# Performance work log

Measured on AMD Instinct MI355X. Metric: run time of the kernel, lower is better.

## Reference

```python
import jax, jax.numpy as jnp
import numpy as np

DIM = 4096
N_HEADS = 32
N_KV_HEADS = 8
HEAD_DIM = 128
WINDOW = 4096
BATCH = 32
START_POS = 4095


def setup_inputs() -> dict:
    key = jax.random.key(0)
    ks = jax.random.split(key, 8)
    x = jax.random.normal(ks[0], (BATCH, DIM), dtype=jnp.float32)
    wqkv = jax.random.normal(ks[1], (DIM, (N_HEADS + 2 * N_KV_HEADS) * HEAD_DIM), dtype=jnp.float32) * 0.02
    wo = jax.random.normal(ks[2], (N_HEADS * HEAD_DIM, DIM), dtype=jnp.float32) * 0.02
    cos = jax.random.uniform(ks[3], (HEAD_DIM,), dtype=jnp.float32)
    sin = jax.random.uniform(ks[4], (HEAD_DIM,), dtype=jnp.float32)
    cache_k = jax.random.normal(ks[5], (BATCH, N_KV_HEADS, WINDOW, HEAD_DIM), dtype=jnp.float32)
    cache_v = jax.random.normal(ks[6], (BATCH, N_KV_HEADS, WINDOW, HEAD_DIM), dtype=jnp.float32)
    mask = jnp.zeros((BATCH, 1, 1, WINDOW), dtype=jnp.float32)
    return {"x": x, "wqkv": wqkv, "wo": wo, "cos": cos, "sin": sin,
            "cache_k": cache_k, "cache_v": cache_v, "mask": mask,
            "start_pos": START_POS}


def _rotate_half(t):
    t1, t2 = jnp.split(t, 2, axis=-1)
    return jnp.concatenate([-t2, t1], axis=-1)


def _rope(t, cos, sin):
    # t: [..., head_dim]; cos/sin: [head_dim] at the current decode position
    return t * cos + _rotate_half(t) * sin


def reference(x, wqkv, wo, cos, sin, cache_k, cache_v, mask, start_pos):
    B, D = x.shape
    KV = cache_k.shape[1]
    Hd = cache_k.shape[3]
    window = cache_k.shape[2]
    H = wo.shape[0] // Hd
    R = H // KV  # GQA repeats
    scale = 1.0 / np.sqrt(Hd)

    # fused QKV projection (matmul_1d + nlp_create_qkv_heads)
    qkv = x @ wqkv  # [B, (H+2*KV)*Hd]
    q = qkv[:, : H * Hd].reshape(B, H, Hd)
    k = qkv[:, H * Hd : (H + KV) * Hd].reshape(B, KV, Hd)
    v = qkv[:, (H + KV) * Hd :].reshape(B, KV, Hd)

    # rotary embedding on q and k at current position
    q = _rope(q, cos, sin)
    k = _rope(k, cos, sin)

    # sliding-window KV cache update at current_pos
    cur = start_pos % window  # python int
    cache_k = cache_k.at[:, :, cur].set(k)
    cache_v = cache_v.at[:, :, cur].set(v)

    # unpad to padded_layer_past_len = min(nearest_32(start_pos+1), window)
    padded_len = min(((start_pos + 1 + 31) // 32) * 32, window)
    keys = cache_k[:, :, :padded_len]   # [B, KV, T, Hd]
    values = cache_v[:, :, :padded_len]

    # grouped-query attention: q -> [B, KV, R, Hd]
    qg = q.reshape(B, KV, R, Hd)
    scores = jnp.einsum("bgrd,bgtd->bgrt", qg, keys) * scale  # [B, KV, R, T]
    scores = scores + mask[:, :, :, :padded_len]  # broadcast over kv-heads/repeats
    attn = jax.nn.softmax(scores, axis=-1)
    out = jnp.einsum("bgrt,bgtd->bgrd", attn, values)  # [B, KV, R, Hd]

    # concat heads + output projection
    out = out.reshape(B, H * Hd)
    return out @ wo  # [B, D]
```

## Files before the change

kernel.cpp:

```cpp
#include <hip/hip_runtime.h>
#include <math.h>

#define DIM 4096
#define NH 32
#define NKV 8
#define HD 128
#define WINDOW 4096
#define BATCH 32
#define QKV_N 6144
#define ATTN_SCALE 0.08838834764831845f
#define WCHUNK 128
#define NCW 32
#define SLICES 16

__device__ __forceinline__ float4 f4max(float4 a, float4 b) {
  return make_float4(fmaxf(a.x, b.x), fmaxf(a.y, b.y), fmaxf(a.z, b.z), fmaxf(a.w, b.w));
}
__device__ __forceinline__ float4 f4add(float4 a, float4 b) {
  return make_float4(a.x + b.x, a.y + b.y, a.z + b.z, a.w + b.w);
}
__device__ __forceinline__ void fma4(float4& a, float4 x, float4 y) {
  a.x = fmaf(x.x, y.x, a.x); a.y = fmaf(x.y, y.y, a.y);
  a.z = fmaf(x.z, y.z, a.z); a.w = fmaf(x.w, y.w, a.w);
}
__device__ __forceinline__ void fma4s(float4& a, float s, float4 v) {
  a.x = fmaf(s, v.x, a.x); a.y = fmaf(s, v.y, a.y);
  a.z = fmaf(s, v.z, a.z); a.w = fmaf(s, v.w, a.w);
}
__device__ __forceinline__ float4 wred_max(float4 v) {
#pragma unroll
  for (int o = 1; o < 64; o <<= 1) {
    v.x = fmaxf(v.x, __shfl_xor(v.x, o));
    v.y = fmaxf(v.y, __shfl_xor(v.y, o));
    v.z = fmaxf(v.z, __shfl_xor(v.z, o));
    v.w = fmaxf(v.w, __shfl_xor(v.w, o));
  }
  return v;
}
__device__ __forceinline__ float4 wred_add(float4 v) {
#pragma unroll
  for (int o = 1; o < 64; o <<= 1) {
    v.x += __shfl_xor(v.x, o);
    v.y += __shfl_xor(v.y, o);
    v.z += __shfl_xor(v.z, o);
    v.w += __shfl_xor(v.w, o);
  }
  return v;
}
__device__ __forceinline__ void xor32_add(float4& v) {
  v.x += __shfl_xor(v.x, 32);
  v.y += __shfl_xor(v.y, 32);
  v.z += __shfl_xor(v.z, 32);
  v.w += __shfl_xor(v.w, 32);
}

template<int N, int K, int NS>
__global__ __launch_bounds__(256)
void gemm_part(const float* __restrict__ x, const float* __restrict__ w,
               float* __restrict__ part) {
  const int t = threadIdx.x;
  const int c0 = blockIdx.x * 64 + (t & 15) * 4;
  const int r0 = (t >> 4) * 2;
  const int kn = K / NS;
  const int ks = blockIdx.y * kn;

  float a00 = 0.f, a01 = 0.f, a02 = 0.f, a03 = 0.f;
  float a10 = 0.f, a11 = 0.f, a12 = 0.f, a13 = 0.f;

  const float* xr0 = x + (size_t)r0 * K;
  const float* xr1 = xr0 + K;
  const float* wp = w + (size_t)ks * N + c0;

  for (int k = ks; k < ks + kn; k += 4) {
    float4 xa = *(const float4*)(xr0 + k);
    float4 xb = *(const float4*)(xr1 + k);
    float xav[4] = {xa.x, xa.y, xa.z, xa.w};
    float xbv[4] = {xb.x, xb.y, xb.z, xb.w};
#pragma unroll
    for (int kk = 0; kk < 4; ++kk) {
      float4 wv = *(const float4*)(wp);
      wp += N;
      a00 = fmaf(xav[kk], wv.x, a00);
      a01 = fmaf(xav[kk], wv.y, a01);
      a02 = fmaf(xav[kk], wv.z, a02);
      a03 = fmaf(xav[kk], wv.w, a03);
      a10 = fmaf(xbv[kk], wv.x, a10);
      a11 = fmaf(xbv[kk], wv.y, a11);
      a12 = fmaf(xbv[kk], wv.z, a12);
      a13 = fmaf(xbv[kk], wv.w, a13);
    }
  }
  float* p = part + ((size_t)blockIdx.y * 32 + r0) * N + c0;
  *(float4*)p = make_float4(a00, a01, a02, a03);
  *(float4*)(p + N) = make_float4(a10, a11, a12, a13);
}

__global__ __launch_bounds__(256)
void rope_reduce(const float* __restrict__ part, const float* __restrict__ cosv,
                 const float* __restrict__ sinv, float* __restrict__ q,
                 float* __restrict__ knew, float* __restrict__ vnew) {
  int idx = blockIdx.x * 256 + threadIdx.x;
  int r = idx / 3072;
  int rem = idx - r * 3072;
  int head = rem >> 6;
  int d = rem & 63;
  int c1 = head * 128 + d;
  int c2 = c1 + 64;
  float v1 = 0.f, v2 = 0.f;
#pragma unroll
  for (int s = 0; s < SLICES; ++s) {
    v1 += part[((size_t)s * 32 + r) * QKV_N + c1];
    v2 += part[((size_t)s * 32 + r) * QKV_N + c2];
  }
  if (head < NH + NKV) {
    float c_lo = cosv[d], c_hi = cosv[d + 64];
    float s_lo = sinv[d], s_hi = sinv[d + 64];
    float o1 = v1 * c_lo - v2 * s_lo;
    float o2 = v2 * c_hi + v1 * s_hi;
    if (head < NH) {
      q[((size_t)r * NH + head) * HD + d] = o1;
      q[((size_t)r * NH + head) * HD + d + 64] = o2;
    } else {
      int g = head - NH;
      knew[((size_t)r * NKV + g) * HD + d] = o1;
      knew[((size_t)r * NKV + g) * HD + d + 64] = o2;
    }
  } else {
    int g = head - NH - NKV;
    vnew[((size_t)r * NKV + g) * HD + d] = v1;
    vnew[((size_t)r * NKV + g) * HD + d + 64] = v2;
  }
}

__global__ __launch_bounds__(256, 5)
void attn_wave(const float* __restrict__ q, const float* __restrict__ knew,
               const float* __restrict__ vnew, const float* __restrict__ cache_k,
               const float* __restrict__ cache_v, const float* __restrict__ mask,
               const int* __restrict__ start_pos_p,
               float* __restrict__ pvp, float* __restrict__ msp) {
  const int bg = blockIdx.x;
  const int b = bg >> 3;
  const int w = threadIdx.x >> 6;
  const int lane = threadIdx.x & 63;
  const int c = blockIdx.y * 4 + w;
  const int sp = start_pos_p[0];
  const int cur = sp & (WINDOW - 1);
  int plen = ((sp + 1 + 31) >> 5) << 5;
  if (plen > WINDOW) plen = WINDOW;
  const int t0 = c * WCHUNK;
  const int tend = min(t0 + WCHUNK, plen);

  const size_t pidx = ((size_t)c * 256 + bg) * 4;
  float* pvb = pvp + pidx * HD;
  float* msb = msp + pidx * 2;

  __shared__ __align__(16) float q_s[4][4 * HD];
  __shared__ __align__(16) float s_s[4][WCHUNK][4];

  if (t0 >= plen) {
    if (lane < 8) msb[lane] = (lane & 1) ? 0.f : -1e30f;
    for (int i = lane; i < 4 * HD; i += 64) pvb[i] = 0.f;
    return;
  }

  {
    const float* qsrc = q + ((size_t)b * NH + (bg & 7) * 4) * HD;
    float4 v0 = *(const float4*)(qsrc + lane * 8);
    float4 v1 = *(const float4*)(qsrc + lane * 8 + 4);
    *(float4*)(&q_s[w][lane * 8]) = v0;
    *(float4*)(&q_s[w][lane * 8 + 4]) = v1;
  }

  const float* kbase = cache_k + (size_t)bg * WINDOW * HD;
  const float* vbase = cache_v + (size_t)bg * WINDOW * HD;
  const float* krow_new = knew + (size_t)bg * HD;
  const float* vrow_new = vnew + (size_t)bg * HD;

  {
    const int p0 = lane >> 2;
    const int dl = lane & 3;
    for (int tt = t0 + p0; tt < t0 + WCHUNK; tt += 16) {
      if (tt < tend) {
        const float* krow = (tt == cur) ? krow_new : (kbase + (size_t)tt * HD);
        float4 a0 = {0,0,0,0}, a1 = {0,0,0,0}, a2 = {0,0,0,0}, a3 = {0,0,0,0};
#pragma unroll
        for (int j = 0; j < 8; ++j) {
          const int f = dl + 4 * j;
          float4 kv = *(const float4*)(krow + 4 * f);
          fma4(a0, kv, *(const float4*)(&q_s[w][0 * HD + 4 * f]));
          fma4(a1, kv, *(const float4*)(&q_s[w][1 * HD + 4 * f]));
          fma4(a2, kv, *(const float4*)(&q_s[w][2 * HD + 4 * f]));
          fma4(a3, kv, *(const float4*)(&q_s[w][3 * HD + 4 * f]));
        }
        float s0 = a0.x + a0.y + a0.z + a0.w;
        float s1 = a1.x + a1.y + a1.z + a1.w;
        float s2 = a2.x + a2.y + a2.z + a2.w;
        float s3 = a3.x + a3.y + a3.z + a3.w;
        s0 += __shfl_xor(s0, 1); s0 += __shfl_xor(s0, 2);
        s1 += __shfl_xor(s1, 1); s1 += __shfl_xor(s1, 2);
        s2 += __shfl_xor(s2, 1); s2 += __shfl_xor(s2, 2);
        s3 += __shfl_xor(s3, 1); s3 += __shfl_xor(s3, 2);
        float sv = (dl == 0) ? s0 : (dl == 1) ? s1 : (dl == 2) ? s2 : s3;
        s_s[w][tt - t0][dl] = sv * ATTN_SCALE + mask[(size_t)b * WINDOW + tt];
      } else {
        s_s[w][tt - t0][dl] = -1e30f;
      }
    }
  }

  float4 r0 = *(const float4*)(s_s[w][lane]);
  float4 r1 = *(const float4*)(s_s[w][lane + 64]);
  float4 mx = wred_max(f4max(r0, r1));
  float4 e0, e1;
  e0.x = __expf(r0.x - mx.x); e0.y = __expf(r0.y - mx.y);
  e0.z = __expf(r0.z - mx.z); e0.w = __expf(r0.w - mx.w);
  e1.x = __expf(r1.x - mx.x); e1.y = __expf(r1.y - mx.y);
  e1.z = __expf(r1.z - mx.z); e1.w = __expf(r1.w - mx.w);
  *(float4*)(s_s[w][lane]) = e0;
  *(float4*)(s_s[w][lane + 64]) = e1;
  float4 sm = wred_add(f4add(e0, e1));
  if (lane == 0) {
    msb[0] = mx.x; msb[1] = sm.x;
    msb[2] = mx.y; msb[3] = sm.y;
    msb[4] = mx.z; msb[5] = sm.z;
    msb[6] = mx.w; msb[7] = sm.w;
  }

  {
    const int d4 = lane & 31;
    const int half = lane >> 5;
    float4 a0 = {0,0,0,0}, a1 = {0,0,0,0}, a2 = {0,0,0,0}, a3 = {0,0,0,0};
    for (int tt = t0 + half; tt < tend; tt += 2) {
      const float* vrow = (tt == cur) ? vrow_new : (vbase + (size_t)tt * HD);
      float4 vv = *(const float4*)(vrow + 4 * d4);
      float4 p = *(const float4*)(s_s[w][tt - t0]);
      fma4s(a0, p.x, vv);
      fma4s(a1, p.y, vv);
      fma4s(a2, p.z, vv);
      fma4s(a3, p.w, vv);
    }
    xor32_add(a0); xor32_add(a1); xor32_add(a2); xor32_add(a3);
    if (half == 0) {
      *(float4*)(&pvb[0 * HD + 4 * d4]) = a0;
      *(float4*)(&pvb[1 * HD + 4 * d4]) = a1;
      *(float4*)(&pvb[2 * HD + 4 * d4]) = a2;
      *(float4*)(&pvb[3 * HD + 4 * d4]) = a3;
    }
  }
}

__global__ __launch_bounds__(256)
void attn_combine(const float* __restrict__ pvp, const float* __restrict__ msp,
                  float* __restrict__ attn_out) {
  int idx = blockIdx.x * 256 + threadIdx.x;
  int b = idx >> 12;
  int rem = idx & 4095;
  int hf = rem >> 7;
  int d = rem & 127;
  int g = hf >> 2, hh = hf & 3;
  int bg = b * 8 + g;
  float M = -1e30f, den = 0.f, num = 0.f;
#pragma unroll 4
  for (int c = 0; c < NCW; ++c) {
    size_t base = ((size_t)c * 256 + bg) * 4 + hh;
    float m = msp[base * 2];
    float s = msp[base * 2 + 1];
    float p = pvp[base * HD + d];
    float Mn = fmaxf(M, m);
    float so = __expf(M - Mn);
    float sn = __expf(m - Mn);
    den = den * so + s * sn;
    num = num * so + p * sn;
    M = Mn;
  }
  attn_out[idx] = num / den;
}

__global__ __launch_bounds__(256)
void reduce_out(const float* __restrict__ part, float* __restrict__ out) {
  int idx = blockIdx.x * 256 + threadIdx.x;
  float s = 0.f;
#pragma unroll
  for (int sl = 0; sl < SLICES; ++sl) s += part[(size_t)sl * 32 * DIM + idx];
  out[idx] = s;
}

extern "C" void kernel_launch(void* const* d_in, const int* in_sizes, int n_in,
                              void* d_out, int out_size, void* d_ws, size_t ws_size,
                              hipStream_t stream) {
  const float* x       = (const float*)d_in[0];
  const float* wqkv    = (const float*)d_in[1];
  const float* wo      = (const float*)d_in[2];
  const float* cosv    = (const float*)d_in[3];
  const float* sinv    = (const float*)d_in[4];
  const float* cache_k = (const float*)d_in[5];
  const float* cache_v = (const float*)d_in[6];
  const float* mask    = (const float*)d_in[7];
  const int*   start_p = (const int*)d_in[8];
  float* ws = (float*)d_ws;

  float* part     = ws;
  float* q        = ws + 3145728;
  float* knew     = q + 131072;
  float* vnew     = knew + 32768;
  float* attn_out = vnew + 32768;
  float* pvp      = attn_out + 131072;
  float* msp      = pvp + 4194304;
  float* out      = (float*)d_out;

  gemm_part<QKV_N, DIM, SLICES><<<dim3(QKV_N / 64, SLICES), 256, 0, stream>>>(x, wqkv, part);
  rope_reduce<<<384, 256, 0, stream>>>(part, cosv, sinv, q, knew, vnew);
  attn_wave<<<dim3(BATCH * NKV, NCW / 4), 256, 0, stream>>>(q, knew, vnew, cache_k,
                                                            cache_v, mask, start_p,
                                                            pvp, msp);
  attn_combine<<<512, 256, 0, stream>>>(pvp, msp, attn_out);
  gemm_part<DIM, DIM, SLICES><<<dim3(DIM / 64, SLICES), 256, 0, stream>>>(attn_out, wo, part);
  reduce_out<<<512, 256, 0, stream>>>(part, out);
}
```

Before: 368.6 us.

## Fuse all stages into one cooperative persistent kernel with grid syncs

Merges the six launches (QKV GEMM, rope reduce, split attention, combine, output GEMM, final reduce) into one persistent cooperative kernel that separates stages with grid-wide syncs, sized from occupancy. The GEMMs are retiled: each block stages a transposed 32x128 slice of x in LDS and computes 32 rows by 256 columns, with 32 K-slices instead of 16. Attention chunks become grid-stride tasks per wavefront. The aim is to remove launch gaps and tail effects between kernels, at the cost of grid-sync overhead, larger partial-sum buffers and possibly lower occupancy. A non-cooperative fallback path is kept.

Result: slower. 529.7 us (+43.7%).

```diff
diff --git a/kernel.cpp b/kernel.cpp
--- a/kernel.cpp
+++ b/kernel.cpp
@@ -1,5 +1,8 @@
 #include <hip/hip_runtime.h>
+#include <hip/hip_cooperative_groups.h>
 #include <math.h>
+
+namespace cg = cooperative_groups;
 
 #define DIM 4096
 #define NH 32
@@ -11,7 +14,12 @@
 #define ATTN_SCALE 0.08838834764831845f
 #define WCHUNK 128
 #define NCW 32
-#define SLICES 16
+#define SL_A 32
+#define SL_E 32
+#define KN 128
+#define TILES_A 768
+#define TILES_E 512
+#define MAX_GRID 1024
 
 __device__ __forceinline__ float4 f4max(float4 a, float4 b) {
   return make_float4(fmaxf(a.x, b.x), fmaxf(a.y, b.y), fmaxf(a.z, b.z), fmaxf(a.w, b.w));
@@ -54,122 +62,101 @@
   v.w += __shfl_xor(v.w, 32);
 }
 
-template<int N, int K, int NS>
-__global__ __launch_bounds__(256)
-void gemm_part(const float* __restrict__ x, const float* __restrict__ w,
-               float* __restrict__ part) {
+template<int N>
+__device__ void gemm_tile(const float* __restrict__ xsrc, const float* __restrict__ w,
+                          float* __restrict__ part, int strip, int slice, float* xT) {
   const int t = threadIdx.x;
-  const int c0 = blockIdx.x * 64 + (t & 15) * 4;
-  const int r0 = (t >> 4) * 2;
-  const int kn = K / NS;
-  const int ks = blockIdx.y * kn;
-
-  float a00 = 0.f, a01 = 0.f, a02 = 0.f, a03 = 0.f;
-  float a10 = 0.f, a11 = 0.f, a12 = 0.f, a13 = 0.f;
-
-  const float* xr0 = x + (size_t)r0 * K;
-  const float* xr1 = xr0 + K;
-  const float* wp = w + (size_t)ks * N + c0;
-
-  for (int k = ks; k < ks + kn; k += 4) {
-    float4 xa = *(const float4*)(xr0 + k);
-    float4 xb = *(const float4*)(xr1 + k);
-    float xav[4] = {xa.x, xa.y, xa.z, xa.w};
-    float xbv[4] = {xb.x, xb.y, xb.z, xb.w};
+  const int c0 = strip * 256;
+  const int ks = slice * KN;
+  for (int lin = t; lin < 32 * 32; lin += 256) {
+    int r = lin >> 5;
+    int c4 = lin & 31;
+    float4 v = *(const float4*)(xsrc + (size_t)r * DIM + ks + 4 * c4);
+    xT[(4 * c4 + 0) * 32 + r] = v.x;
+    xT[(4 * c4 + 1) * 32 + r] = v.y;
+    xT[(4 * c4 + 2) * 32 + r] = v.z;
+    xT[(4 * c4 + 3) * 32 + r] = v.w;
+  }
+  __syncthreads();
+
+  const int l = t & 63;
+  const int r0 = (t >> 6) * 8;
+  float4 acc[8];
 #pragma unroll
-    for (int kk = 0; kk < 4; ++kk) {
-      float4 wv = *(const float4*)(wp);
-      wp += N;
-      a00 = fmaf(xav[kk], wv.x, a00);
-      a01 = fmaf(xav[kk], wv.y, a01);
-      a02 = fmaf(xav[kk], wv.z, a02);
-      a03 = fmaf(xav[kk], wv.w, a03);
-      a10 = fmaf(xbv[kk], wv.x, a10);
-      a11 = fmaf(xbv[kk], wv.y, a11);
-      a12 = fmaf(xbv[kk], wv.z, a12);
-      a13 = fmaf(xbv[kk], wv.w, a13);
-    }
-  }
-  float* p = part + ((size_t)blockIdx.y * 32 + r0) * N + c0;
-  *(float4*)p = make_float4(a00, a01, a02, a03);
-  *(float4*)(p + N) = make_float4(a10, a11, a12, a13);
-}
-
-__global__ __launch_bounds__(256)
-void rope_reduce(const float* __restrict__ part, const float* __restrict__ cosv,
-                 const float* __restrict__ sinv, float* __restrict__ q,
-                 float* __restrict__ knew, float* __restrict__ vnew) {
-  int idx = blockIdx.x * 256 + threadIdx.x;
-  int r = idx / 3072;
-  int rem = idx - r * 3072;
-  int head = rem >> 6;
-  int d = rem & 63;
-  int c1 = head * 128 + d;
-  int c2 = c1 + 64;
-  float v1 = 0.f, v2 = 0.f;
+  for (int i = 0; i < 8; ++i) acc[i] = make_float4(0.f, 0.f, 0.f, 0.f);
+
+  const float* wp = w + (size_t)ks * N + c0 + 4 * l;
+  for (int k = 0; k < KN; ++k) {
+    float4 wv = *(const float4*)wp;
+    wp += N;
+    float4 xa = *(const float4*)(&xT[k * 32 + r0]);
+    float4 xb = *(const float4*)(&xT[k * 32 + r0 + 4]);
+    fma4s(acc[0], xa.x, wv); fma4s(acc[1], xa.y, wv);
+    fma4s(acc[2], xa.z, wv); fma4s(acc[3], xa.w, wv);
+    fma4s(acc[4], xb.x, wv); fma4s(acc[5], xb.y, wv);
+    fma4s(acc[6], xb.z, wv); fma4s(acc[7], xb.w, wv);
+  }
+  float* p = part + ((size_t)slice * 32 + r0) * N + c0 + 4 * l;
 #pragma unroll
-  for (int s = 0; s < SLICES; ++s) {
-    v1 += part[((size_t)s * 32 + r) * QKV_N + c1];
-    v2 += part[((size_t)s * 32 + r) * QKV_N + c2];
-  }
-  if (head < NH + NKV) {
-    float c_lo = cosv[d], c_hi = cosv[d + 64];
-    float s_lo = sinv[d], s_hi = sinv[d + 64];
-    float o1 = v1 * c_lo - v2 * s_lo;
-    float o2 = v2 * c_hi + v1 * s_hi;
-    if (head < NH) {
-      q[((size_t)r * NH + head) * HD + d] = o1;
-      q[((size_t)r * NH + head) * HD + d + 64] = o2;
+  for (int i = 0; i < 8; ++i) *(float4*)(p + (size_t)i * N) = acc[i];
+  __syncthreads();
+}
+
+__device__ void stageB(int blk, int nblk, const float* __restrict__ part,
+                       const float* __restrict__ cosv, const float* __restrict__ sinv,
+                       float* __restrict__ q, float* __restrict__ knew,
+                       float* __restrict__ vnew) {
+  for (int idx = blk * 256 + threadIdx.x; idx < 32 * 48 * 64; idx += nblk * 256) {
+    int r = idx / 3072;
+    int rem = idx - r * 3072;
+    int head = rem >> 6;
+    int d = rem & 63;
+    int c1 = head * 128 + d;
+    int c2 = c1 + 64;
+    float v1 = 0.f, v2 = 0.f;
+#pragma unroll 8
+    for (int s = 0; s < SL_A; ++s) {
+      v1 += part[((size_t)s * 32 + r) * QKV_N + c1];
+      v2 += part[((size_t)s * 32 + r) * QKV_N + c2];
+    }
+    if (head < NH + NKV) {
+      float c_lo = cosv[d], c_hi = cosv[d + 64];
+      float s_lo = sinv[d], s_hi = sinv[d + 64];
+      float o1 = v1 * c_lo - v2 * s_lo;
+      float o2 = v2 * c_hi + v1 * s_hi;
+      if (head < NH) {
+        q[((size_t)r * NH + head) * HD + d] = o1;
+        q[((size_t)r * NH + head) * HD + d + 64] = o2;
+      } else {
+        int g = head - NH;
+        knew[((size_t)r * NKV + g) * HD + d] = o1;
+        knew[((size_t)r * NKV + g) * HD + d + 64] = o2;
+      }
     } else {
-      int g = head - NH;
-      knew[((size_t)r * NKV + g) * HD + d] = o1;
-      knew[((size_t)r * NKV + g) * HD + d + 64] = o2;
-    }
-  } else {
-    int g = head - NH - NKV;
-    vnew[((size_t)r * NKV + g) * HD + d] = v1;
-    vnew[((size_t)r * NKV + g) * HD + d + 64] = v2;
-  }
-}
-
-__global__ __launch_bounds__(256, 5)
-void attn_wave(const float* __restrict__ q, const float* __restrict__ knew,
-               const float* __restrict__ vnew, const float* __restrict__ cache_k,
-               const float* __restrict__ cache_v, const float* __restrict__ mask,
-               const int* __restrict__ start_pos_p,
-               float* __restrict__ pvp, float* __restrict__ msp) {
-  const int bg = blockIdx.x;
+      int g = head - NH - NKV;
+      vnew[((size_t)r * NKV + g) * HD + d] = v1;
+      vnew[((size_t)r * NKV + g) * HD + d + 64] = v2;
+    }
+  }
+}
+
+__device__ void stageC(int blk, int nblk, const float* __restrict__ q,
+                       const float* __restrict__ knew, const float* __restrict__ vnew,
+                       const float* __restrict__ cache_k, const float* __restrict__ cache_v,
+                       const float* __restrict__ mask, const int* __restrict__ start_pos_p,
+                       float* __restrict__ pvp, float* __restrict__ msp, float* LDS) {
+  const int t = threadIdx.x;
+  const int w = t >> 6, lane = t & 63;
+  float* q_s = LDS + w * 512;
+  float* s_s = LDS + 2048 + w * 512;
+  const int gw0 = blk * 4 + w;
+  const int nw = nblk * 4;
+  const int bg = gw0 & 255;
   const int b = bg >> 3;
-  const int w = threadIdx.x >> 6;
-  const int lane = threadIdx.x & 63;
-  const int c = blockIdx.y * 4 + w;
   const int sp = start_pos_p[0];
   const int cur = sp & (WINDOW - 1);
   int plen = ((sp + 1 + 31) >> 5) << 5;
   if (plen > WINDOW) plen = WINDOW;
-  const int t0 = c * WCHUNK;
-  const int tend = min(t0 + WCHUNK, plen);
-
-  const size_t pidx = ((size_t)c * 256 + bg) * 4;
-  float* pvb = pvp + pidx * HD;
-  float* msb = msp + pidx * 2;
-
-  __shared__ __align__(16) float q_s[4][4 * HD];
-  __shared__ __align__(16) float s_s[4][WCHUNK][4];
-
-  if (t0 >= plen) {
-    if (lane < 8) msb[lane] = (lane & 1) ? 0.f : -1e30f;
-    for (int i = lane; i < 4 * HD; i += 64) pvb[i] = 0.f;
-    return;
-  }
-
-  {
-    const float* qsrc = q + ((size_t)b * NH + (bg & 7) * 4) * HD;
-    float4 v0 = *(const float4*)(qsrc + lane * 8);
-    float4 v1 = *(const float4*)(qsrc + lane * 8 + 4);
-    *(float4*)(&q_s[w][lane * 8]) = v0;
-    *(float4*)(&q_s[w][lane * 8 + 4]) = v1;
-  }
 
   const float* kbase = cache_k + (size_t)bg * WINDOW * HD;
   const float* vbase = cache_v + (size_t)bg * WINDOW * HD;
@@ -177,112 +164,198 @@
   const float* vrow_new = vnew + (size_t)bg * HD;
 
   {
-    const int p0 = lane >> 2;
-    const int dl = lane & 3;
-    for (int tt = t0 + p0; tt < t0 + WCHUNK; tt += 16) {
-      if (tt < tend) {
-        const float* krow = (tt == cur) ? krow_new : (kbase + (size_t)tt * HD);
-        float4 a0 = {0,0,0,0}, a1 = {0,0,0,0}, a2 = {0,0,0,0}, a3 = {0,0,0,0};
+    const float* qsrc = q + ((size_t)b * NH + (bg & 7) * 4) * HD;
+    *(float4*)(&q_s[lane * 8]) = *(const float4*)(qsrc + lane * 8);
+    *(float4*)(&q_s[lane * 8 + 4]) = *(const float4*)(qsrc + lane * 8 + 4);
+  }
+
+  for (int task = gw0; task < NCW * 256; task += nw) {
+    const int c = task >> 8;
+    const int t0 = c * WCHUNK;
+    const int tend = min(t0 + WCHUNK, plen);
+    const size_t pidx = ((size_t)c * 256 + bg) * 4;
+    float* pvb = pvp + pidx * HD;
+    float* msb = msp + pidx * 2;
+
+    if (t0 >= plen) {
+      if (lane < 8) msb[lane] = (lane & 1) ? 0.f : -1e30f;
+      for (int i = lane; i < 4 * HD; i += 64) pvb[i] = 0.f;
+      continue;
+    }
+
+    {
+      const int p0 = lane >> 2;
+      const int dl = lane & 3;
+      for (int tt = t0 + p0; tt < t0 + WCHUNK; tt += 16) {
+        if (tt < tend) {
+          const float* krow = (tt == cur) ? krow_new : (kbase + (size_t)tt * HD);
+          float4 a0 = {0,0,0,0}, a1 = {0,0,0,0}, a2 = {0,0,0,0}, a3 = {0,0,0,0};
 #pragma unroll
-        for (int j = 0; j < 8; ++j) {
-          const int f = dl + 4 * j;
-          float4 kv = *(const float4*)(krow + 4 * f);
-          fma4(a0, kv, *(const float4*)(&q_s[w][0 * HD + 4 * f]));
-          fma4(a1, kv, *(const float4*)(&q_s[w][1 * HD + 4 * f]));
-          fma4(a2, kv, *(const float4*)(&q_s[w][2 * HD + 4 * f]));
-          fma4(a3, kv, *(const float4*)(&q_s[w][3 * HD + 4 * f]));
+          for (int j = 0; j < 8; ++j) {
+            const int f = dl + 4 * j;
+            float4 kv = *(const float4*)(krow + 4 * f);
+            fma4(a0, kv, *(const float4*)(&q_s[0 * HD + 4 * f]));
+            fma4(a1, kv, *(const float4*)(&q_s[1 * HD + 4 * f]));
+            fma4(a2, kv, *(const float4*)(&q_s[2 * HD + 4 * f]));
+            fma4(a3, kv, *(const float4*)(&q_s[3 * HD + 4 * f]));
+          }
+          float s0 = a0.x + a0.y + a0.z + a0.w;
+          float s1 = a1.x + a1.y + a1.z + a1.w;
+          float s2 = a2.x + a2.y + a2.z + a2.w;
+          float s3 = a3.x + a3.y + a3.z + a3.w;
+          s0 += __shfl_xor(s0, 1); s0 += __shfl_xor(s0, 2);
+          s1 += __shfl_xor(s1, 1); s1 += __shfl_xor(s1, 2);
+          s2 += __shfl_xor(s2, 1); s2 += __shfl_xor(s2, 2);
+          s3 += __shfl_xor(s3, 1); s3 += __shfl_xor(s3, 2);
+          float sv = (dl == 0) ? s0 : (dl == 1) ? s1 : (dl == 2) ? s2 : s3;
+          s_s[(tt - t0) * 4 + dl] = sv * ATTN_SCALE + mask[(size_t)b * WINDOW + tt];
+        } else {
+          s_s[(tt - t0) * 4 + dl] = -1e30f;
         }
-        float s0 = a0.x + a0.y + a0.z + a0.w;
-        float s1 = a1.x + a1.y + a1.z + a1.w;
-        float s2 = a2.x + a2.y + a2.z + a2.w;
-        float s3 = a3.x + a3.y + a3.z + a3.w;
-        s0 += __shfl_xor(s0, 1); s0 += __shfl_xor(s0, 2);
-        s1 += __shfl_xor(s1, 1); s1 += __shfl_xor(s1, 2);
-        s2 += __shfl_xor(s2, 1); s2 += __shfl_xor(s2, 2);
-        s3 += __shfl_xor(s3, 1); s3 += __shfl_xor(s3, 2);
-        float sv = (dl == 0) ? s0 : (dl == 1) ? s1 : (dl == 2) ? s2 : s3;
-        s_s[w][tt - t0][dl] = sv * ATTN_SCALE + mask[(size_t)b * WINDOW + tt];
-      } else {
-        s_s[w][tt - t0][dl] = -1e30f;
       }
     }
-  }
-
-  float4 r0 = *(const float4*)(s_s[w][lane]);
-  float4 r1 = *(const float4*)(s_s[w][lane + 64]);
-  float4 mx = wred_max(f4max(r0, r1));
-  float4 e0, e1;
-  e0.x = __expf(r0.x - mx.x); e0.y = __expf(r0.y - mx.y);
-  e0.z = __expf(r0.z - mx.z); e0.w = __expf(r0.w - mx.w);
-  e1.x = __expf(r1.x - mx.x); e1.y = __expf(r1.y - mx.y);
-  e1.z = __expf(r1.z - mx.z); e1.w = __expf(r1.w - mx.w);
-  *(float4*)(s_s[w][lane]) = e0;
-  *(float4*)(s_s[w][lane + 64]) = e1;
-  float4 sm = wred_add(f4add(e0, e1));
-  if (lane == 0) {
-    msb[0] = mx.x; msb[1] = sm.x;
-    msb[2] = mx.y; msb[3] = sm.y;
-    msb[4] = mx.z; msb[5] = sm.z;
-    msb[6] = mx.w; msb[7] = sm.w;
-  }
-
-  {
-    const int d4 = lane & 31;
-    const int half = lane >> 5;
-    float4 a0 = {0,0,0,0}, a1 = {0,0,0,0}, a2 = {0,0,0,0}, a3 = {0,0,0,0};
-    for (int tt = t0 + half; tt < tend; tt += 2) {
-      const float* vrow = (tt == cur) ? vrow_new : (vbase + (size_t)tt * HD);
-      float4 vv = *(const float4*)(vrow + 4 * d4);
-      float4 p = *(const float4*)(s_s[w][tt - t0]);
-      fma4s(a0, p.x, vv);
-      fma4s(a1, p.y, vv);
-      fma4s(a2, p.z, vv);
-      fma4s(a3, p.w, vv);
-    }
-    xor32_add(a0); xor32_add(a1); xor32_add(a2); xor32_add(a3);
-    if (half == 0) {
-      *(float4*)(&pvb[0 * HD + 4 * d4]) = a0;
-      *(float4*)(&pvb[1 * HD + 4 * d4]) = a1;
-      *(float4*)(&pvb[2 * HD + 4 * d4]) = a2;
-      *(float4*)(&pvb[3 * HD + 4 * d4]) = a3;
-    }
-  }
-}
-
-__global__ __launch_bounds__(256)
-void attn_combine(const float* __restrict__ pvp, const float* __restrict__ msp,
-                  float* __restrict__ attn_out) {
-  int idx = blockIdx.x * 256 + threadIdx.x;
-  int b = idx >> 12;
-  int rem = idx & 4095;
-  int hf = rem >> 7;
-  int d = rem & 127;
-  int g = hf >> 2, hh = hf & 3;
-  int bg = b * 8 + g;
-  float M = -1e30f, den = 0.f, num = 0.f;
+    float4 r0v = *(const float4*)(&s_s[lane * 4]);
+    float4 r1v = *(const float4*)(&s_s[(lane + 64) * 4]);
+    float4 mx = wred_max(f4max(r0v, r1v));
+    float4 e0, e1;
+    e0.x = __expf(r0v.x - mx.x); e0.y = __expf(r0v.y - mx.y);
+    e0.z = __expf(r0v.z - mx.z); e0.w = __expf(r0v.w - mx.w);
+    e1.x = __expf(r1v.x - mx.x); e1.y = __expf(r1v.y - mx.y);
+    e1.z = __expf(r1v.z - mx.z); e1.w = __expf(r1v.w - mx.w);
+    *(float4*)(&s_s[lane * 4]) = e0;
+    *(float4*)(&s_s[(lane + 64) * 4]) = e1;
+    float4 sm = wred_add(f4add(e0, e1));
+    if (lane == 0) {
+      msb[0] = mx.x; msb[1] = sm.x;
+      msb[2] = mx.y; msb[3] = sm.y;
+      msb[4] = mx.z; msb[5] = sm.z;
+      msb[6] = mx.w; msb[7] = sm.w;
+    }
+    {
+      const int d4 = lane & 31;
+      const int half = lane >> 5;
+      float4 a0 = {0,0,0,0}, a1 = {0,0,0,0}, a2 = {0,0,0,0}, a3 = {0,0,0,0};
+      for (int tt = t0 + half; tt < tend; tt += 2) {
+        const float* vrow = (tt == cur) ? vrow_new : (vbase + (size_t)tt * HD);
+        float4 vv = *(const float4*)(vrow + 4 * d4);
+        float4 p = *(const float4*)(&s_s[(tt - t0) * 4]);
+        fma4s(a0, p.x, vv);
+        fma4s(a1, p.y, vv);
+        fma4s(a2, p.z, vv);
+        fma4s(a3, p.w, vv);
+      }
+      xor32_add(a0); xor32_add(a1); xor32_add(a2); xor32_add(a3);
+      if (half == 0) {
+        *(float4*)(&pvb[0 * HD + 4 * d4]) = a0;
+        *(float4*)(&pvb[1 * HD + 4 * d4]) = a1;
+        *(float4*)(&pvb[2 * HD + 4 * d4]) = a2;
+        *(float4*)(&pvb[3 * HD + 4 * d4]) = a3;
+      }
+    }
+  }
+}
+
+__device__ void stageD(int blk, int nblk, const float* __restrict__ pvp,
+                       const float* __restrict__ msp, float* __restrict__ attn_out) {
+  for (int idx = blk * 256 + threadIdx.x; idx < BATCH * DIM; idx += nblk * 256) {
+    int b = idx >> 12;
+    int rem = idx & 4095;
+    int hf = rem >> 7;
+    int d = rem & 127;
+    int g = hf >> 2, hh = hf & 3;
+    int bg = b * 8 + g;
+    float M = -1e30f, den = 0.f, num = 0.f;
 #pragma unroll 4
-  for (int c = 0; c < NCW; ++c) {
-    size_t base = ((size_t)c * 256 + bg) * 4 + hh;
-    float m = msp[base * 2];
-    float s = msp[base * 2 + 1];
-    float p = pvp[base * HD + d];
-    float Mn = fmaxf(M, m);
-    float so = __expf(M - Mn);
-    float sn = __expf(m - Mn);
-    den = den * so + s * sn;
-    num = num * so + p * sn;
-    M = Mn;
-  }
-  attn_out[idx] = num / den;
-}
-
-__global__ __launch_bounds__(256)
-void reduce_out(const float* __restrict__ part, float* __restrict__ out) {
-  int idx = blockIdx.x * 256 + threadIdx.x;
-  float s = 0.f;
-#pragma unroll
-  for (int sl = 0; sl < SLICES; ++sl) s += part[(size_t)sl * 32 * DIM + idx];
-  out[idx] = s;
+    for (int c = 0; c < NCW; ++c) {
+      size_t base = ((size_t)c * 256 + bg) * 4 + hh;
+      float m = msp[base * 2];
+      float s = msp[base * 2 + 1];
+      float p = pvp[base * HD + d];
+      float Mn = fmaxf(M, m);
+      float so = __expf(M - Mn);
+      float sn = __expf(m - Mn);
+      den = den * so + s * sn;
+      num = num * so + p * sn;
+      M = Mn;
+    }
+    attn_out[idx] = num / den;
+  }
+}
+
+__device__ void stageF(int blk, int nblk, const float* __restrict__ partE,
+                       float* __restrict__ out) {
+  for (int idx = blk * 256 + threadIdx.x; idx < BATCH * DIM; idx += nblk * 256) {
+    float s = 0.f;
+#pragma unroll 8
+    for (int sl = 0; sl < SL_E; ++sl) s += partE[(size_t)sl * BATCH * DIM + idx];
+    out[idx] = s;
+  }
+}
+
+__global__ __launch_bounds__(256, 4)
+void fused_kernel(const float* __restrict__ x, const float* __restrict__ wqkv,
+                  const float* __restrict__ wo, const float* __restrict__ cosv,
+                  const float* __restrict__ sinv, const float* __restrict__ cache_k,
+                  const float* __restrict__ cache_v, const float* __restrict__ mask,
+                  const int* __restrict__ start_pos_p,
+                  float* partA, float* q, float* knew, float* vnew,
+                  float* attn_out, float* pvp, float* msp, float* partE,
+                  float* out) {
+  cg::grid_group grid = cg::this_grid();
+  const int blk = blockIdx.x;
+  const int nblk = gridDim.x;
+  __shared__ __align__(16) float LDS[4096];
+
+  for (int tile = blk; tile < TILES_A; tile += nblk)
+    gemm_tile<QKV_N>(x, wqkv, partA, tile % 24, tile / 24, LDS);
+  grid.sync();
+
+  stageB(blk, nblk, partA, cosv, sinv, q, knew, vnew);
+  grid.sync();
+
+  stageC(blk, nblk, q, knew, vnew, cache_k, cache_v, mask, start_pos_p, pvp, msp, LDS);
+  grid.sync();
+
+  stageD(blk, nblk, pvp, msp, attn_out);
+  grid.sync();
+
+  for (int tile = blk; tile < TILES_E; tile += nblk)
+    gemm_tile<DIM>(attn_out, wo, partE, tile & 15, tile >> 4, LDS);
+  grid.sync();
+
+  stageF(blk, nblk, partE, out);
+}
+
+__global__ __launch_bounds__(256)
+void k_gemmA(const float* __restrict__ x, const float* __restrict__ wqkv, float* partA) {
+  __shared__ __align__(16) float LDS[4096];
+  gemm_tile<QKV_N>(x, wqkv, partA, blockIdx.x % 24, blockIdx.x / 24, LDS);
+}
+__global__ __launch_bounds__(256)
+void k_rope(const float* part, const float* cosv, const float* sinv,
+            float* q, float* knew, float* vnew) {
+  stageB(blockIdx.x, gridDim.x, part, cosv, sinv, q, knew, vnew);
+}
+__global__ __launch_bounds__(256)
+void k_attn(const float* q, const float* knew, const float* vnew,
+            const float* cache_k, const float* cache_v, const float* mask,
+            const int* start_pos_p, float* pvp, float* msp) {
+  __shared__ __align__(16) float LDS[4096];
+  stageC(blockIdx.x, gridDim.x, q, knew, vnew, cache_k, cache_v, mask,
+         start_pos_p, pvp, msp, LDS);
+}
+__global__ __launch_bounds__(256)
+void k_combine(const float* pvp, const float* msp, float* attn_out) {
+  stageD(blockIdx.x, gridDim.x, pvp, msp, attn_out);
+}
+__global__ __launch_bounds__(256)
+void k_gemmE(const float* attn_out, const float* wo, float* partE) {
+  __shared__ __align__(16) float LDS[4096];
+  gemm_tile<DIM>(attn_out, wo, partE, blockIdx.x & 15, blockIdx.x >> 4, LDS);
+}
+__global__ __launch_bounds__(256)
+void k_reduce(const float* partE, float* out) {
+  stageF(blockIdx.x, gridDim.x, partE, out);
 }
 
 extern "C" void kernel_launch(void* const* d_in, const int* in_sizes, int n_in,
@@ -299,21 +372,47 @@
   const int*   start_p = (const int*)d_in[8];
   float* ws = (float*)d_ws;
 
-  float* part     = ws;
-  float* q        = ws + 3145728;
+  float* partA    = ws;
+  float* q        = ws + 6291456;
   float* knew     = q + 131072;
   float* vnew     = knew + 32768;
   float* attn_out = vnew + 32768;
   float* pvp      = attn_out + 131072;
   float* msp      = pvp + 4194304;
+  float* partE    = msp + 65536;
   float* out      = (float*)d_out;
 
-  gemm_part<QKV_N, DIM, SLICES><<<dim3(QKV_N / 64, SLICES), 256, 0, stream>>>(x, wqkv, part);
-  rope_reduce<<<384, 256, 0, stream>>>(part, cosv, sinv, q, knew, vnew);
-  attn_wave<<<dim3(BATCH * NKV, NCW / 4), 256, 0, stream>>>(q, knew, vnew, cache_k,
-                                                            cache_v, mask, start_p,
-                                                            pvp, msp);
-  attn_combine<<<512, 256, 0, stream>>>(pvp, msp, attn_out);
-  gemm_part<DIM, DIM, SLICES><<<dim3(DIM / 64, SLICES), 256, 0, stream>>>(attn_out, wo, part);
-  reduce_out<<<512, 256, 0, stream>>>(part, out);
-}
+  int nblk = 0;
+  {
+    int dev = 0, ncu = 0, occ = 0;
+    if (hipGetDevice(&dev) == hipSuccess &&
+        hipDeviceGetAttribute(&ncu, hipDeviceAttributeMultiprocessorCount, dev) == hipSuccess &&
+        hipOccupancyMaxActiveBlocksPerMultiprocessor(&occ, (const void*)fused_kernel,
+                                                     256, 0) == hipSuccess) {
+      long n = (long)ncu * (long)occ;
+      if (n > MAX_GRID) n = MAX_GRID;
+      n -= (n % 64);
+      if (n >= 256) nblk = (int)n;
+    }
+  }
+
+  bool launched = false;
+  if (nblk > 0) {
+    void* args[] = {(void*)&x, (void*)&wqkv, (void*)&wo, (void*)&cosv, (void*)&sinv,
+                    (void*)&cache_k, (void*)&cache_v, (void*)&mask, (void*)&start_p,
+                    (void*)&partA, (void*)&q, (void*)&knew, (void*)&vnew,
+                    (void*)&attn_out, (void*)&pvp, (void*)&msp, (void*)&partE,
+                    (void*)&out};
+    launched = (hipLaunchCooperativeKernel((const void*)fused_kernel, dim3(nblk),
+                                           dim3(256), args, 0, stream) == hipSuccess);
+  }
+  if (!launched) {
+    k_gemmA<<<TILES_A, 256, 0, stream>>>(x, wqkv, partA);
+    k_rope<<<384, 256, 0, stream>>>(partA, cosv, sinv, q, knew, vnew);
+    k_attn<<<2048, 256, 0, stream>>>(q, knew, vnew, cache_k, cache_v, mask,
+                                     start_p, pvp, msp);
+    k_combine<<<512, 256, 0, stream>>>(pvp, msp, attn_out);
+    k_gemmE<<<TILES_E, 256, 0, stream>>>(attn_out, wo, partE);
+    k_reduce<<<512, 256, 0, stream>>>(partE, out);
+  }
+}
```
